# Performance work log

Hardware: AMD Instinct MI355X
Metric: run time of the kernel (lower is better)

## Reference

```python
import jax, jax.numpy as jnp
import numpy as np

EMBED = 128
HEADS = 32          # embed_dim // 4, forced by fuse Conv2d channel counts
HEAD_DIM = EMBED // HEADS  # 4
WS = (4, 7, 7)
N = WS[0] * WS[1] * WS[2]  # 196 tokens per window
B = 64              # batch * num_windows
SCALE = HEAD_DIM ** -0.5
EPS = 1e-5


def _rel_index():
    d, h, w = WS
    coords = np.stack(np.meshgrid(np.arange(d), np.arange(h), np.arange(w), indexing='ij'))
    flat = coords.reshape(3, -1)                       # [3, N]
    rel = (flat[:, :, None] - flat[:, None, :]).transpose(1, 2, 0).astype(np.int64)  # [N,N,3]
    rel[:, :, 0] += d - 1
    rel[:, :, 1] += h - 1
    rel[:, :, 2] += w - 1
    rel[:, :, 0] *= (2 * h - 1) * (2 * w - 1)
    rel[:, :, 1] *= (2 * w - 1)
    return rel.sum(-1).astype(np.int32)                # [N, N]


def setup_inputs() -> dict:
    key = jax.random.key(0)
    ks = jax.random.split(key, 7)
    d, h, w = WS
    tbl = (2 * d - 1) * (2 * h - 1) * (2 * w - 1)
    return {
        'x_in':      jax.random.normal(ks[0], (B, N, EMBED), dtype=jnp.float32),
        'x_in2':     jax.random.normal(ks[1], (B, N, EMBED), dtype=jnp.float32),
        'qkv_w':     jax.random.normal(ks[2], (3 * EMBED, EMBED), dtype=jnp.float32) * 0.02,
        'proj_w':    jax.random.normal(ks[3], (EMBED, EMBED), dtype=jnp.float32) * 0.02,
        'proj_b':    jnp.zeros((EMBED,), dtype=jnp.float32),
        'rpb_table': jax.random.normal(ks[4], (tbl, HEADS), dtype=jnp.float32) * 0.02,
        'fuse_w':    jax.random.normal(ks[5], (EMBED // 4, EMBED // 2), dtype=jnp.float32) * 0.1,
        'fuse_b':    jnp.zeros((EMBED // 4,), dtype=jnp.float32),
        'rel_idx':   jnp.asarray(_rel_index()),
    }


def _branch(x, qkv_w):
    b, n, c = x.shape
    qkv = (x @ qkv_w.T).reshape(b, n, 3, HEADS, c // HEADS).transpose(2, 0, 3, 1, 4)
    q, k, v = qkv[0] * SCALE, qkv[1], qkv[2]           # [b, H, n, d]
    attn = jnp.einsum('bhnd,bhmd->bhnm', q, k)         # [b, H, n, n]
    return attn, v


def reference(x_in, x_in2, qkv_w, proj_w, proj_b, rpb_table, fuse_w, fuse_b, rel_idx):
    b, n, c = x_in.shape
    attn1, v1 = _branch(x_in, qkv_w)
    attn2, v2 = _branch(x_in2, qkv_w)

    # conv-gated value fusion: Conv2d 1x1 over channel dim (= 2H) + InstanceNorm2d + ReLU + Sigmoid
    vcat = jnp.concatenate([v1, v2], axis=1)           # [b, 2H, n, d]
    v = jnp.einsum('bcnd,oc->bond', vcat, fuse_w) + fuse_b[None, :, None, None]  # [b, H, n, d]
    mu = v.mean(axis=(2, 3), keepdims=True)
    var = v.var(axis=(2, 3), keepdims=True)            # biased, as InstanceNorm2d
    v = (v - mu) * jax.lax.rsqrt(var + EPS)
    v = jax.nn.sigmoid(jax.nn.relu(v))

    # relative position bias: gather [n*n] rows of table -> [H, n, n]
    bias = rpb_table[rel_idx[:n, :n].reshape(-1)].reshape(n, n, HEADS).transpose(2, 0, 1)

    attn = jax.nn.softmax(attn1 + attn2 + bias[None], axis=-1)  # [b, H, n, n]
    x = jnp.einsum('bhnm,bhmd->bhnd', attn, v).transpose(0, 2, 1, 3).reshape(b, n, c)
    return x @ proj_w.T + proj_b
```

## Files before the change

### kernel.cpp

```cpp
#include <hip/hip_runtime.h>
#include <hip/hip_bf16.h>
#include <stdint.h>

#define NB   64
#define NTOK 196
#define NH   32
#define HD   4
#define CE   128
#define NM   38416

typedef __bf16 bf16x8 __attribute__((ext_vector_type(8)));
typedef short  bf16x4s __attribute__((ext_vector_type(4)));
typedef float  f32x4  __attribute__((ext_vector_type(4)));

#define QSCALE 0.7213475204444817f
#define LOG2E  1.4426950408889634f

__device__ __forceinline__ float u2f(unsigned short u) {
    union { unsigned int i; float f; } z;
    z.i = ((unsigned int)u) << 16;
    return z.f;
}
__device__ __forceinline__ unsigned short f2u(float f) {
    union { float f; unsigned int i; } z; z.f = f;
    unsigned int x = z.i;
    return (unsigned short)((x + 0x7fffu + ((x >> 16) & 1u)) >> 16);
}

extern "C" __global__ __launch_bounds__(256) void qkv_bias(
    const float* __restrict__ x1,
    const float* __restrict__ x2,
    const float* __restrict__ qkvw,
    const int* __restrict__ rel_idx, const float* __restrict__ rpb,
    unsigned short* __restrict__ Qb, unsigned short* __restrict__ Kb,
    unsigned short* __restrict__ V, unsigned short* __restrict__ biasM)
{
    __shared__ alignas(16) unsigned short AT[64][136];
    __shared__ alignas(16) unsigned short BT[64][136];
    const int tid = threadIdx.x;

    if (blockIdx.y == 6) {
        const int bx = blockIdx.x;
        const int qt = bx % 13, h = bx / 13;
        const int lane = tid & 63, wv = tid >> 6;
        const int quad = lane >> 4, tc = lane & 15;
        for (int nt = wv; nt < 14; nt += 4) {
            union { uint2 v; unsigned short s[4]; } e;
#pragma unroll
            for (int r = 0; r < 4; ++r) {
                int q   = qt * 16 + tc;
                int key = nt * 16 + quad * 4 + r;
                unsigned short u = 0xFF80;
                if (q < 196 && key < 196) {
                    int idx = rel_idx[q * 196 + key];
                    u = f2u(rpb[idx * 32 + h] * LOG2E);
                }
                e.s[r] = u;
            }
            unsigned int off = (((h * 13 + qt) * 7 + (nt >> 1)) * 64 + lane) * 8
                               + (nt & 1) * 4;
            *(uint2*)(biasM + off) = e.v;
        }
        return;
    }
    if (blockIdx.x >= 392) return;

    const int r0 = blockIdx.x * 64;
    const int j0 = blockIdx.y * 64;

    for (int idx = tid; idx < 2048; idx += 256) {
        int row = idx >> 5, k0 = (idx & 31) << 2;
        int r = r0 + row;
        const float* xp = (r >= 12544) ? x2 : x1;
        int rem = r - ((r >= 12544) ? 12544 : 0);
        float4 v = *(const float4*)&xp[rem * 128 + k0];
        ushort4 u; u.x = f2u(v.x); u.y = f2u(v.y); u.z = f2u(v.z); u.w = f2u(v.w);
        *(ushort4*)&AT[row][k0] = u;
    }
    for (int idx = tid; idx < 2048; idx += 256) {
        int row = idx >> 5, k0 = (idx & 31) << 2;
        float4 v = *(const float4*)&qkvw[(j0 + row) * 128 + k0];
        ushort4 u; u.x = f2u(v.x); u.y = f2u(v.y); u.z = f2u(v.z); u.w = f2u(v.w);
        *(ushort4*)&BT[row][k0] = u;
    }
    __syncthreads();

    const int lane = tid & 63, w = tid >> 6;
    const int wj = (w >> 1) * 32;
    const int wt = (w & 1) * 32;
    const int quad = lane >> 4, tc = lane & 15;

    f32x4 acc[2][2] = {};
#pragma unroll
    for (int ks = 0; ks < 4; ++ks) {
        int k0 = ks * 32 + quad * 8;
        bf16x8 a0 = *(const bf16x8*)&BT[wj + tc][k0];
        bf16x8 a1 = *(const bf16x8*)&BT[wj + 16 + tc][k0];
        bf16x8 b0 = *(const bf16x8*)&AT[wt + tc][k0];
        bf16x8 b1 = *(const bf16x8*)&AT[wt + 16 + tc][k0];
        acc[0][0] = __builtin_amdgcn_mfma_f32_16x16x32_bf16(a0, b0, acc[0][0], 0, 0, 0);
        acc[0][1] = __builtin_amdgcn_mfma_f32_16x16x32_bf16(a0, b1, acc[0][1], 0, 0, 0);
        acc[1][0] = __builtin_amdgcn_mfma_f32_16x16x32_bf16(a1, b0, acc[1][0], 0, 0, 0);
        acc[1][1] = __builtin_amdgcn_mfma_f32_16x16x32_bf16(a1, b1, acc[1][1], 0, 0, 0);
    }

    const int sel = j0 >> 7;
#pragma unroll
    for (int mi = 0; mi < 2; ++mi) {
        int jbase = (j0 + wj + mi * 16 + quad * 4) & 127;
        int hh = jbase >> 2;
#pragma unroll
        for (int ni = 0; ni < 2; ++ni) {
            int tok = r0 + wt + ni * 16 + tc;
            int branch = (tok >= 12544) ? 1 : 0;
            int rem = tok - branch * 12544;
            int bb = rem / 196;
            int nn = rem - bb * 196;
            union { uint2 v; unsigned short s[4]; } pk2;
            if (sel == 0) {
#pragma unroll
                for (int r = 0; r < 4; ++r) pk2.s[r] = f2u(acc[mi][ni][r] * QSCALE);
                *(uint2*)&Qb[((bb * 32 + hh) * 196 + nn) * 8 + branch * 4] = pk2.v;
            } else if (sel == 1) {
#pragma unroll
                for (int r = 0; r < 4; ++r) pk2.s[r] = f2u(acc[mi][ni][r]);
                *(uint2*)&Kb[((bb * 32 + hh) * 196 + nn) * 8 + branch * 4] = pk2.v;
            } else {
#pragma unroll
                for (int r = 0; r < 4; ++r) pk2.s[r] = f2u(acc[mi][ni][r]);
                *(uint2*)&V[(bb * 64 + branch * 32 + hh) * 784 + nn * 4] = pk2.v;
            }
        }
    }
}

__device__ __forceinline__ float block_sum(float v, float* red, int tid) {
#pragma unroll
    for (int off = 32; off > 0; off >>= 1) v += __shfl_down(v, off);
    __syncthreads();
    if ((tid & 63) == 0) red[tid >> 6] = v;
    __syncthreads();
    return red[0] + red[1] + red[2] + red[3];
}

__device__ __forceinline__ float act_sig_relu(float x) {
    return x > 0.f ? __fdividef(1.f, 1.f + __expf(-x)) : 0.5f;
}

extern "C" __global__ __launch_bounds__(256) void fuse_kernel(
    const unsigned short* __restrict__ V,
    const float* __restrict__ fuse_w,
    const float* __restrict__ fuse_b,
    float* __restrict__ Vf)
{
    const int b = blockIdx.x, o0 = blockIdx.y * 4;
    const int tid = threadIdx.x;
    __shared__ float fws[4][64];
    __shared__ float red[4];
    fws[tid >> 6][tid & 63] = fuse_w[(o0 + (tid >> 6)) * 64 + (tid & 63)];
    __syncthreads();

    const bool act = tid < 196;
    const unsigned short* Vb = V + b * 64 * 784 + tid * 4;
    float4 a[4] = {};
    for (int c = 0; c < 64; ++c) {
        float4 x = {0.f, 0.f, 0.f, 0.f};
        if (act) {
            uint2 u = *(const uint2*)(Vb + c * 784);
            union { unsigned int i; float f; } z;
            z.i = u.x << 16;          x.x = z.f;
            z.i = u.x & 0xffff0000u;  x.y = z.f;
            z.i = u.y << 16;          x.z = z.f;
            z.i = u.y & 0xffff0000u;  x.w = z.f;
        }
#pragma unroll
        for (int o = 0; o < 4; ++o) {
            float w0 = fws[o][c];
            a[o].x = fmaf(w0, x.x, a[o].x);
            a[o].y = fmaf(w0, x.y, a[o].y);
            a[o].z = fmaf(w0, x.z, a[o].z);
            a[o].w = fmaf(w0, x.w, a[o].w);
        }
    }

    const float inv784 = 1.0f / 784.0f;
#pragma unroll
    for (int o = 0; o < 4; ++o) {
        float fb0 = fuse_b[o0 + o];
        float4 v = a[o];
        if (act) { v.x += fb0; v.y += fb0; v.z += fb0; v.w += fb0; }
        float s = v.x + v.y + v.z + v.w;
        float q = v.x*v.x + v.y*v.y + v.z*v.z + v.w*v.w;
        float S = block_sum(s, red, tid);
        float Q = block_sum(q, red, tid);
        float mu = S * inv784;
        float rstd = rsqrtf(Q * inv784 - mu * mu + 1e-5f);
        if (act) {
            float4 o4;
            o4.x = act_sig_relu((v.x - mu) * rstd);
            o4.y = act_sig_relu((v.y - mu) * rstd);
            o4.z = act_sig_relu((v.z - mu) * rstd);
            o4.w = act_sig_relu((v.w - mu) * rstd);
            *(float4*)&Vf[(b * 32 + o0 + o) * 784 + tid * 4] = o4;
        }
    }
}

extern "C" __global__ __launch_bounds__(256) void attn_kernel(
    const unsigned short* __restrict__ Qb, const unsigned short* __restrict__ Kb,
    const float* __restrict__ Vf, const unsigned short* __restrict__ biasM,
    unsigned short* __restrict__ Ob)
{
    const int bh = blockIdx.x;
    const int b = bh >> 5, h = bh & 31;
    __shared__ alignas(16) unsigned short Qs[208][8];
    __shared__ alignas(16) unsigned short Ks[224][8];
    __shared__ alignas(16) unsigned short VT[16][232];
    const int tid = threadIdx.x;

    const unsigned short* Qrow = Qb + bh * 196 * 8;
    const unsigned short* Krow = Kb + bh * 196 * 8;
    if (tid < 208) {
        uint4 z = {0, 0, 0, 0};
        uint4 v = (tid < 196) ? *(const uint4*)(Qrow + tid * 8) : z;
        *(uint4*)&Qs[tid][0] = v;
    }
    if (tid < 224) {
        uint4 z = {0, 0, 0, 0};
        uint4 v = (tid < 196) ? *(const uint4*)(Krow + tid * 8) : z;
        *(uint4*)&Ks[tid][0] = v;
    }
    {
        unsigned int* vtw = (unsigned int*)&VT[0][0];
        for (int i = tid; i < (16 * 232) / 2; i += 256) vtw[i] = 0u;
    }
    __syncthreads();
    if (tid < 196) {
        float4 vv = *(const float4*)(Vf + bh * 784 + tid * 4);
        VT[0][tid] = f2u(vv.x); VT[1][tid] = f2u(vv.y);
        VT[2][tid] = f2u(vv.z); VT[3][tid] = f2u(vv.w);
        VT[4][tid] = 0x3F80;
    }
    __syncthreads();

    const int lane = tid & 63, wv = tid >> 6;
    const int quad = lane >> 4, tc = lane & 15;

    bf16x4s vfr16[14];
#pragma unroll
    for (int t = 0; t < 14; ++t)
        vfr16[t] = *(const bf16x4s*)&VT[tc][t * 16 + quad * 4];

    const unsigned short* bias_h = biasM + (unsigned)(h * 13) * 3584;

    for (int qt = wv; qt < 13; qt += 4) {
        bf16x8 bq = {};
        if (quad == 0) bq = *(const bf16x8*)&Qs[qt * 16 + tc][0];
        const unsigned short* bias_q = bias_h + qt * 3584;
        uint4 bw[7];
#pragma unroll
        for (int kt = 0; kt < 7; ++kt)
            bw[kt] = *(const uint4*)(bias_q + kt * 512 + lane * 8);
        f32x4 O0 = {}, O1 = {};
#pragma unroll
        for (int kt = 0; kt < 7; ++kt) {
            f32x4 s0, s1;
            {
                union { unsigned int u; float f; } c;
                c.u = bw[kt].x << 16;          s0[0] = c.f;
                c.u = bw[kt].x & 0xffff0000u;  s0[1] = c.f;
                c.u = bw[kt].y << 16;          s0[2] = c.f;
                c.u = bw[kt].y & 0xffff0000u;  s0[3] = c.f;
                c.u = bw[kt].z << 16;          s1[0] = c.f;
                c.u = bw[kt].z & 0xffff0000u;  s1[1] = c.f;
                c.u = bw[kt].w << 16;          s1[2] = c.f;
                c.u = bw[kt].w & 0xffff0000u;  s1[3] = c.f;
            }
            bf16x8 ka0 = *(const bf16x8*)&Ks[(kt * 2 + 0) * 16 + tc][0];
            bf16x8 ka1 = *(const bf16x8*)&Ks[(kt * 2 + 1) * 16 + tc][0];
            s0 = __builtin_amdgcn_mfma_f32_16x16x32_bf16(ka0, bq, s0, 0, 0, 0);
            s1 = __builtin_amdgcn_mfma_f32_16x16x32_bf16(ka1, bq, s1, 0, 0, 0);
            float e0 = __builtin_amdgcn_exp2f(s0[0]);
            float e1 = __builtin_amdgcn_exp2f(s0[1]);
            float e2 = __builtin_amdgcn_exp2f(s0[2]);
            float e3 = __builtin_amdgcn_exp2f(s0[3]);
            float g0 = __builtin_amdgcn_exp2f(s1[0]);
            float g1 = __builtin_amdgcn_exp2f(s1[1]);
            float g2 = __builtin_amdgcn_exp2f(s1[2]);
            float g3 = __builtin_amdgcn_exp2f(s1[3]);
            union { int d[2]; bf16x4s v; } pf0, pf1;
            pf0.d[0] = (int)__builtin_amdgcn_perm(__float_as_uint(e1), __float_as_uint(e0), 0x07060302u);
            pf0.d[1] = (int)__builtin_amdgcn_perm(__float_as_uint(e3), __float_as_uint(e2), 0x07060302u);
            pf1.d[0] = (int)__builtin_amdgcn_perm(__float_as_uint(g1), __float_as_uint(g0), 0x07060302u);
            pf1.d[1] = (int)__builtin_amdgcn_perm(__float_as_uint(g3), __float_as_uint(g2), 0x07060302u);
            O0 = __builtin_amdgcn_mfma_f32_16x16x16bf16_1k(vfr16[kt * 2 + 0], pf0.v, O0, 0, 0, 0);
            O1 = __builtin_amdgcn_mfma_f32_16x16x16bf16_1k(vfr16[kt * 2 + 1], pf1.v, O1, 0, 0, 0);
        }
        f32x4 Oacc;
        Oacc[0] = O0[0] + O1[0];
        Oacc[1] = O0[1] + O1[1];
        Oacc[2] = O0[2] + O1[2];
        Oacc[3] = O0[3] + O1[3];
        float rs = __shfl(Oacc[0], 16 + tc);
        int q = qt * 16 + tc;
        if (quad == 0 && q < 196) {
            float inv = __builtin_amdgcn_rcpf(rs);
            union { uint2 v; unsigned short s[4]; } pk2;
            pk2.s[0] = f2u(Oacc[0] * inv);
            pk2.s[1] = f2u(Oacc[1] * inv);
            pk2.s[2] = f2u(Oacc[2] * inv);
            pk2.s[3] = f2u(Oacc[3] * inv);
            *(uint2*)&Ob[(b * 196 + q) * 128 + h * 4] = pk2.v;
        }
    }
}

extern "C" __global__ __launch_bounds__(256) void proj_kernel(
    const unsigned short* __restrict__ Ob, const float* __restrict__ projw,
    const float* __restrict__ projb, float* __restrict__ out)
{
    __shared__ alignas(16) unsigned short AT[64][136];
    __shared__ alignas(16) unsigned short BT[64][136];
    const int tid = threadIdx.x;
    const int r0 = blockIdx.x * 64;
    const int j0 = blockIdx.y * 64;

    for (int idx = tid; idx < 1024; idx += 256) {
        int row = idx >> 4, k0 = (idx & 15) << 3;
        *(uint4*)&AT[row][k0] = *(const uint4*)&Ob[(r0 + row) * 128 + k0];
    }
    for (int idx = tid; idx < 2048; idx += 256) {
        int row = idx >> 5, k0 = (idx & 31) << 2;
        float4 v = *(const float4*)&projw[(j0 + row) * 128 + k0];
        ushort4 u; u.x = f2u(v.x); u.y = f2u(v.y); u.z = f2u(v.z); u.w = f2u(v.w);
        *(ushort4*)&BT[row][k0] = u;
    }
    __syncthreads();

    const int lane = tid & 63, w = tid >> 6;
    const int wm = (w >> 1) * 32, wn = (w & 1) * 32;
    const int quad = lane >> 4, tcol = lane & 15;

    f32x4 acc[2][2] = {};
#pragma unroll
    for (int ks = 0; ks < 4; ++ks) {
        int k0 = ks * 32 + quad * 8;
        bf16x8 a0 = *(const bf16x8*)&AT[wm + tcol][k0];
        bf16x8 a1 = *(const bf16x8*)&AT[wm + 16 + tcol][k0];
        bf16x8 b0 = *(const bf16x8*)&BT[wn + tcol][k0];
        bf16x8 b1 = *(const bf16x8*)&BT[wn + 16 + tcol][k0];
        acc[0][0] = __builtin_amdgcn_mfma_f32_16x16x32_bf16(a0, b0, acc[0][0], 0, 0, 0);
        acc[0][1] = __builtin_amdgcn_mfma_f32_16x16x32_bf16(a0, b1, acc[0][1], 0, 0, 0);
        acc[1][0] = __builtin_amdgcn_mfma_f32_16x16x32_bf16(a1, b0, acc[1][0], 0, 0, 0);
        acc[1][1] = __builtin_amdgcn_mfma_f32_16x16x32_bf16(a1, b1, acc[1][1], 0, 0, 0);
    }

#pragma unroll
    for (int mi = 0; mi < 2; ++mi) {
#pragma unroll
        for (int ni = 0; ni < 2; ++ni) {
            int j = j0 + wn + ni * 16 + tcol;
            float pb = projb[j];
#pragma unroll
            for (int reg = 0; reg < 4; ++reg) {
                int r = r0 + wm + mi * 16 + quad * 4 + reg;
                out[r * 128 + j] = acc[mi][ni][reg] + pb;
            }
        }
    }
}

extern "C" void kernel_launch(void* const* d_in, const int* in_sizes, int n_in,
                              void* d_out, int out_size, void* d_ws, size_t ws_size,
                              hipStream_t stream)
{
    const float* x1    = (const float*)d_in[0];
    const float* x2    = (const float*)d_in[1];
    const float* qkvw  = (const float*)d_in[2];
    const float* projw = (const float*)d_in[3];
    const float* projb = (const float*)d_in[4];
    const float* rpb   = (const float*)d_in[5];
    const float* fw    = (const float*)d_in[6];
    const float* fb    = (const float*)d_in[7];
    const int*   rel   = (const int*)d_in[8];
    float* out = (float*)d_out;

    char* w = (char*)d_ws;
    unsigned short* Qb  = (unsigned short*)(w);
    unsigned short* Kb  = (unsigned short*)(w + 6422528);
    unsigned short* V   = (unsigned short*)(w + 12845056);
    float*          Vf  = (float*)(w + 19267584);
    unsigned short* bM  = (unsigned short*)(w + 25690112);
    unsigned short* Ob  = (unsigned short*)(w + 28672000);

    qkv_bias  <<<dim3(416, 7), dim3(256), 0, stream>>>(x1, x2, qkvw, rel, rpb,
                                                       Qb, Kb, V, bM);
    fuse_kernel<<<dim3(64, 8),  dim3(256), 0, stream>>>(V, fw, fb, Vf);
    attn_kernel<<<dim3(2048),   dim3(256), 0, stream>>>(Qb, Kb, Vf, bM, Ob);
    proj_kernel<<<dim3(196, 2), dim3(256), 0, stream>>>(Ob, projw, projb, out);
}
```

Measured before the change: 155.1 us.

## Store fused V as transposed bf16 and interleave all query tiles per key tile

The fuse kernel now writes the gated V as bf16 in a transposed [d][n] layout, which halves that intermediate and lets the attention kernel copy it straight into shared memory with no per-element conversion. The attention kernel swaps loop order: each wave holds up to four query tiles with separate accumulators and walks the key tiles once, so each K and V fragment is read from LDS once per key tile instead of once per query tile. This exposes more independent MFMA chains per step. In exchange register pressure rises, bias loads are issued inside the loop, and out-of-range query tiles are clamped, which adds redundant compute for waves that have fewer than four valid tiles.

After: 156.0 us. Within noise of the previous version (+0.6%).

```diff
diff --git a/kernel.cpp b/kernel.cpp
--- a/kernel.cpp
+++ b/kernel.cpp
@@ -151,7 +151,7 @@
     const unsigned short* __restrict__ V,
     const float* __restrict__ fuse_w,
     const float* __restrict__ fuse_b,
-    float* __restrict__ Vf)
+    unsigned short* __restrict__ VfT)
 {
     const int b = blockIdx.x, o0 = blockIdx.y * 4;
     const int tid = threadIdx.x;
@@ -196,19 +196,18 @@
         float mu = S * inv784;
         float rstd = rsqrtf(Q * inv784 - mu * mu + 1e-5f);
         if (act) {
-            float4 o4;
-            o4.x = act_sig_relu((v.x - mu) * rstd);
-            o4.y = act_sig_relu((v.y - mu) * rstd);
-            o4.z = act_sig_relu((v.z - mu) * rstd);
-            o4.w = act_sig_relu((v.w - mu) * rstd);
-            *(float4*)&Vf[(b * 32 + o0 + o) * 784 + tid * 4] = o4;
+            unsigned short* op = VfT + (unsigned)(b * 32 + o0 + o) * 784 + tid;
+            op[0 * 196] = f2u(act_sig_relu((v.x - mu) * rstd));
+            op[1 * 196] = f2u(act_sig_relu((v.y - mu) * rstd));
+            op[2 * 196] = f2u(act_sig_relu((v.z - mu) * rstd));
+            op[3 * 196] = f2u(act_sig_relu((v.w - mu) * rstd));
         }
     }
 }
 
 extern "C" __global__ __launch_bounds__(256) void attn_kernel(
     const unsigned short* __restrict__ Qb, const unsigned short* __restrict__ Kb,
-    const float* __restrict__ Vf, const unsigned short* __restrict__ biasM,
+    const unsigned short* __restrict__ VfT, const unsigned short* __restrict__ biasM,
     unsigned short* __restrict__ Ob)
 {
     const int bh = blockIdx.x;
@@ -218,8 +217,8 @@
     __shared__ alignas(16) unsigned short VT[16][232];
     const int tid = threadIdx.x;
 
-    const unsigned short* Qrow = Qb + bh * 196 * 8;
-    const unsigned short* Krow = Kb + bh * 196 * 8;
+    const unsigned short* Qrow = Qb + bh * 1568;
+    const unsigned short* Krow = Kb + bh * 1568;
     if (tid < 208) {
         uint4 z = {0, 0, 0, 0};
         uint4 v = (tid < 196) ? *(const uint4*)(Qrow + tid * 8) : z;
@@ -232,54 +231,59 @@
     }
     {
         unsigned int* vtw = (unsigned int*)&VT[0][0];
-        for (int i = tid; i < (16 * 232) / 2; i += 256) vtw[i] = 0u;
+        for (int i = tid; i < 580; i += 256) vtw[i] = 0u;
     }
     __syncthreads();
     if (tid < 196) {
-        float4 vv = *(const float4*)(Vf + bh * 784 + tid * 4);
-        VT[0][tid] = f2u(vv.x); VT[1][tid] = f2u(vv.y);
-        VT[2][tid] = f2u(vv.z); VT[3][tid] = f2u(vv.w);
-        VT[4][tid] = 0x3F80;
-    }
+        uint2 u = ((const uint2*)(VfT + (unsigned)bh * 784))[tid];
+        int d = tid / 49;
+        int n = (tid - d * 49) * 4;
+        *(uint2*)&VT[d][n] = u;
+    }
+    if (tid < 98) *(unsigned int*)&VT[4][tid * 2] = 0x3F803F80u;
     __syncthreads();
 
     const int lane = tid & 63, wv = tid >> 6;
     const int quad = lane >> 4, tc = lane & 15;
 
-    bf16x4s vfr16[14];
-#pragma unroll
-    for (int t = 0; t < 14; ++t)
-        vfr16[t] = *(const bf16x4s*)&VT[tc][t * 16 + quad * 4];
+    bf16x8 bq[4];
+#pragma unroll
+    for (int i = 0; i < 4; ++i) {
+        int qt = wv + 4 * i;
+        int qtc = qt > 12 ? 12 : qt;
+        bf16x8 z = {};
+        bq[i] = z;
+        if (quad == 0) bq[i] = *(const bf16x8*)&Qs[qtc * 16 + tc][0];
+    }
 
     const unsigned short* bias_h = biasM + (unsigned)(h * 13) * 3584;
-
-    for (int qt = wv; qt < 13; qt += 4) {
-        bf16x8 bq = {};
-        if (quad == 0) bq = *(const bf16x8*)&Qs[qt * 16 + tc][0];
-        const unsigned short* bias_q = bias_h + qt * 3584;
-        uint4 bw[7];
-#pragma unroll
-        for (int kt = 0; kt < 7; ++kt)
-            bw[kt] = *(const uint4*)(bias_q + kt * 512 + lane * 8);
-        f32x4 O0 = {}, O1 = {};
-#pragma unroll
-        for (int kt = 0; kt < 7; ++kt) {
+    f32x4 O[4] = {};
+
+#pragma unroll 2
+    for (int kt = 0; kt < 7; ++kt) {
+        bf16x8 ka0 = *(const bf16x8*)&Ks[(kt * 2 + 0) * 16 + tc][0];
+        bf16x8 ka1 = *(const bf16x8*)&Ks[(kt * 2 + 1) * 16 + tc][0];
+        bf16x4s vf0 = *(const bf16x4s*)&VT[tc][(kt * 2 + 0) * 16 + quad * 4];
+        bf16x4s vf1 = *(const bf16x4s*)&VT[tc][(kt * 2 + 1) * 16 + quad * 4];
+#pragma unroll
+        for (int i = 0; i < 4; ++i) {
+            int qt = wv + 4 * i;
+            int qtc = qt > 12 ? 12 : qt;
+            uint4 bw = *(const uint4*)(bias_h + qtc * 3584 + kt * 512 + lane * 8);
             f32x4 s0, s1;
             {
                 union { unsigned int u; float f; } c;
-                c.u = bw[kt].x << 16;          s0[0] = c.f;
-                c.u = bw[kt].x & 0xffff0000u;  s0[1] = c.f;
-                c.u = bw[kt].y << 16;          s0[2] = c.f;
-                c.u = bw[kt].y & 0xffff0000u;  s0[3] = c.f;
-                c.u = bw[kt].z << 16;          s1[0] = c.f;
-                c.u = bw[kt].z & 0xffff0000u;  s1[1] = c.f;
-                c.u = bw[kt].w << 16;          s1[2] = c.f;
-                c.u = bw[kt].w & 0xffff0000u;  s1[3] = c.f;
+                c.u = bw.x << 16;          s0[0] = c.f;
+                c.u = bw.x & 0xffff0000u;  s0[1] = c.f;
+                c.u = bw.y << 16;          s0[2] = c.f;
+                c.u = bw.y & 0xffff0000u;  s0[3] = c.f;
+                c.u = bw.z << 16;          s1[0] = c.f;
+                c.u = bw.z & 0xffff0000u;  s1[1] = c.f;
+                c.u = bw.w << 16;          s1[2] = c.f;
+                c.u = bw.w & 0xffff0000u;  s1[3] = c.f;
             }
-            bf16x8 ka0 = *(const bf16x8*)&Ks[(kt * 2 + 0) * 16 + tc][0];
-            bf16x8 ka1 = *(const bf16x8*)&Ks[(kt * 2 + 1) * 16 + tc][0];
-            s0 = __builtin_amdgcn_mfma_f32_16x16x32_bf16(ka0, bq, s0, 0, 0, 0);
-            s1 = __builtin_amdgcn_mfma_f32_16x16x32_bf16(ka1, bq, s1, 0, 0, 0);
+            s0 = __builtin_amdgcn_mfma_f32_16x16x32_bf16(ka0, bq[i], s0, 0, 0, 0);
+            s1 = __builtin_amdgcn_mfma_f32_16x16x32_bf16(ka1, bq[i], s1, 0, 0, 0);
             float e0 = __builtin_amdgcn_exp2f(s0[0]);
             float e1 = __builtin_amdgcn_exp2f(s0[1]);
             float e2 = __builtin_amdgcn_exp2f(s0[2]);
@@ -293,23 +297,22 @@
             pf0.d[1] = (int)__builtin_amdgcn_perm(__float_as_uint(e3), __float_as_uint(e2), 0x07060302u);
             pf1.d[0] = (int)__builtin_amdgcn_perm(__float_as_uint(g1), __float_as_uint(g0), 0x07060302u);
             pf1.d[1] = (int)__builtin_amdgcn_perm(__float_as_uint(g3), __float_as_uint(g2), 0x07060302u);
-            O0 = __builtin_amdgcn_mfma_f32_16x16x16bf16_1k(vfr16[kt * 2 + 0], pf0.v, O0, 0, 0, 0);
-            O1 = __builtin_amdgcn_mfma_f32_16x16x16bf16_1k(vfr16[kt * 2 + 1], pf1.v, O1, 0, 0, 0);
-        }
-        f32x4 Oacc;
-        Oacc[0] = O0[0] + O1[0];
-        Oacc[1] = O0[1] + O1[1];
-        Oacc[2] = O0[2] + O1[2];
-        Oacc[3] = O0[3] + O1[3];
-        float rs = __shfl(Oacc[0], 16 + tc);
-        int q = qt * 16 + tc;
+            O[i] = __builtin_amdgcn_mfma_f32_16x16x16bf16_1k(vf0, pf0.v, O[i], 0, 0, 0);
+            O[i] = __builtin_amdgcn_mfma_f32_16x16x16bf16_1k(vf1, pf1.v, O[i], 0, 0, 0);
+        }
+    }
+
+#pragma unroll
+    for (int i = 0; i < 4; ++i) {
+        float rs = __shfl(O[i][0], 16 + tc);
+        int q = (wv + 4 * i) * 16 + tc;
         if (quad == 0 && q < 196) {
             float inv = __builtin_amdgcn_rcpf(rs);
             union { uint2 v; unsigned short s[4]; } pk2;
-            pk2.s[0] = f2u(Oacc[0] * inv);
-            pk2.s[1] = f2u(Oacc[1] * inv);
-            pk2.s[2] = f2u(Oacc[2] * inv);
-            pk2.s[3] = f2u(Oacc[3] * inv);
+            pk2.s[0] = f2u(O[i][0] * inv);
+            pk2.s[1] = f2u(O[i][1] * inv);
+            pk2.s[2] = f2u(O[i][2] * inv);
+            pk2.s[3] = f2u(O[i][3] * inv);
             *(uint2*)&Ob[(b * 196 + q) * 128 + h * 4] = pk2.v;
         }
     }
@@ -389,13 +392,13 @@
     unsigned short* Qb  = (unsigned short*)(w);
     unsigned short* Kb  = (unsigned short*)(w + 6422528);
     unsigned short* V   = (unsigned short*)(w + 12845056);
-    float*          Vf  = (float*)(w + 19267584);
-    unsigned short* bM  = (unsigned short*)(w + 25690112);
-    unsigned short* Ob  = (unsigned short*)(w + 28672000);
+    unsigned short* VfT = (unsigned short*)(w + 19267584);
+    unsigned short* bM  = (unsigned short*)(w + 22478848);
+    unsigned short* Ob  = (unsigned short*)(w + 25460736);
 
     qkv_bias  <<<dim3(416, 7), dim3(256), 0, stream>>>(x1, x2, qkvw, rel, rpb,
                                                        Qb, Kb, V, bM);
-    fuse_kernel<<<dim3(64, 8),  dim3(256), 0, stream>>>(V, fw, fb, Vf);
-    attn_kernel<<<dim3(2048),   dim3(256), 0, stream>>>(Qb, Kb, Vf, bM, Ob);
+    fuse_kernel<<<dim3(64, 8),  dim3(256), 0, stream>>>(V, fw, fb, VfT);
+    attn_kernel<<<dim3(2048),   dim3(256), 0, stream>>>(Qb, Kb, VfT, bM, Ob);
     proj_kernel<<<dim3(196, 2), dim3(256), 0, stream>>>(Ob, projw, projb, out);
 }
```
